# Kernel optimization log

Measured on AMD Instinct MI355X. Metric: run time of the kernel, lower is better.

The kernel has to match this reference:

```python
import jax, jax.numpy as jnp
import numpy as np

H, D = 16, 64  # num_head, num_out
LN_EPS = 1e-5

def setup_inputs() -> dict:
    key = jax.random.key(0)
    ks = jax.random.split(key, 6)
    B, S, C = 4, 2048, 1024
    sc = 0.02
    return {
        "x": jax.random.normal(ks[0], (B, S, C), jnp.float32),
        "mask": jax.random.randint(ks[1], (B, S), 0, 2, jnp.int32),
        "Wq": jax.random.normal(ks[2], (C, C), jnp.float32) * sc,
        "Wk": jax.random.normal(ks[3], (C, C), jnp.float32) * sc,
        "Wv": jax.random.normal(ks[4], (C, C), jnp.float32) * sc,
        "Wr": jax.random.normal(ks[5], (C, C), jnp.float32) * sc,
        "gamma": jnp.ones((C,), jnp.float32),
        "beta": jnp.zeros((C,), jnpip := jnp.float32) if False else jnp.zeros((C,), jnp.float32),
    }

def reference(x, mask, Wq, Wk, Wv, Wr, gamma, beta):
    B, S, C = x.shape
    # torch Linear: y = x @ W.T ; split(num_out,-1) == reshape (B,S,H,D)
    q = (x @ Wq.T).reshape(B, S, H, D)
    k = (x @ Wk.T).reshape(B, S, H, D)
    v = (x @ Wv.T).reshape(B, S, H, D)
    scores = jnp.einsum("bqhd,bkhd->bhqk", q, k) / jnp.sqrt(jnp.float32(D))
    # mask [B,S] over keys; masked positions -> -1e9 (matches masked_fill)
    scores = jnp.where((mask == 0)[:, None, None, :], jnp.float32(-1e9), scores)
    attn = jax.nn.softmax(scores, axis=-1)
    out = jnp.einsum("bhqk,bkhd->bqhd", attn, v).reshape(B, S, H * D)
    out = jax.nn.relu(out + x @ Wr.T)
    mu = jnp.mean(out, axis=-1, keepdims=True)
    var = jnp.mean(jnp.square(out - mu), axis=-1, keepdims=True)
    return (out - mu) / jnp.sqrt(var + LN_EPS) * gamma + beta
```

## Files before the change

kernel.cpp:

```cpp
#include <hip/hip_runtime.h>

typedef __attribute__((ext_vector_type(8))) short short8;
typedef __attribute__((ext_vector_type(8))) unsigned short u16x8;
typedef __attribute__((ext_vector_type(4))) float f32x4;
typedef __attribute__((ext_vector_type(4))) unsigned short u16x4;
typedef __attribute__((ext_vector_type(4))) float float4v;

#define MFMA(a, b, c) __builtin_amdgcn_mfma_f32_16x16x32_bf16(a, b, c, 0, 0, 0)
#define GLOAD_LDS16(gp, lp) __builtin_amdgcn_global_load_lds( \
    (const __attribute__((address_space(1))) void*)(gp),      \
    (__attribute__((address_space(3))) void*)(lp), 16, 0, 0)

__device__ __forceinline__ float bf2f(unsigned short u) {
    union { unsigned int i; float f; } v; v.i = ((unsigned int)u) << 16; return v.f;
}
__device__ __forceinline__ unsigned short f2bf(float f) {
    union { float f; unsigned int i; } v; v.f = f;
    unsigned int r = (v.i + 0x7FFFu + ((v.i >> 16) & 1u)) >> 16;
    return (unsigned short)r;
}
__device__ __forceinline__ unsigned short f2bfr(float f) {
    union { float f; unsigned int i; } v; v.f = f;
    return (unsigned short)((v.i + 0x8000u) >> 16);
}

__global__ __launch_bounds__(256)
void mask_scan(const int* __restrict__ mask, int* __restrict__ kidx, int* __restrict__ seff)
{
    constexpr int S = 2048;
    const int b = blockIdx.x;
    const int tid = threadIdx.x;
    __shared__ int ps[256];
    const int* m = mask + b * S;
    int loc[8], s = 0;
#pragma unroll
    for (int j = 0; j < 8; ++j) { loc[j] = m[tid * 8 + j]; s += loc[j]; }
#pragma unroll
    for (int j = 0; j < 8; ++j) kidx[b * S + tid * 8 + j] = b * S;
    ps[tid] = s;
    __syncthreads();
    for (int off = 1; off < 256; off <<= 1) {
        int v = (tid >= off) ? ps[tid - off] : 0;
        __syncthreads();
        ps[tid] += v;
        __syncthreads();
    }
    int run = (tid > 0) ? ps[tid - 1] : 0;
#pragma unroll
    for (int j = 0; j < 8; ++j) {
        if (loc[j]) kidx[b * S + run] = b * S + tid * 8 + j;
        run += loc[j];
    }
    if (tid == 255) seff[b] = ps[255];
}

__global__ __launch_bounds__(256)
void ingest_all(const float* __restrict__ X,
                const float* __restrict__ Wq, const float* __restrict__ Wk,
                const float* __restrict__ Wv, const float* __restrict__ Wr,
                unsigned short* __restrict__ dst)
{
    constexpr int X4 = 2097152;
    constexpr int T4 = X4 + 4 * 262144;
    const int stride = gridDim.x * blockDim.x;
    for (int i = blockIdx.x * blockDim.x + threadIdx.x; i < T4; i += stride) {
        const float* src;
        int off;
        if (i < X4) { src = X; off = i; }
        else {
            int jj = i - X4;
            int ws = jj >> 18;
            off = jj & 0x3FFFF;
            src = (ws == 0) ? Wq : (ws == 1) ? Wk : (ws == 2) ? Wv : Wr;
        }
        float4v v = ((const float4v*)src)[off];
        u16x4 o;
#pragma unroll
        for (int j = 0; j < 4; ++j) o[j] = f2bf(v[j]);
        ((u16x4*)dst)[i] = o;
    }
}

__global__ __launch_bounds__(256)
void proj_gemm(const unsigned short* __restrict__ X,
               const unsigned short* __restrict__ Wq, const unsigned short* __restrict__ Wk,
               const unsigned short* __restrict__ Wv, const unsigned short* __restrict__ Wr,
               unsigned short* __restrict__ Qo, unsigned short* __restrict__ Ko,
               unsigned short* __restrict__ Vo, unsigned short* __restrict__ Ro,
               const int* __restrict__ kidx, const int* __restrict__ seff)
{
    constexpr int Kd = 1024, N = 1024;
    __shared__ unsigned short smem[128 * 136];
    unsigned short* As = smem;
    unsigned short* Bs = smem + 4096;
    unsigned short* Ct = smem;
    const int tid = threadIdx.x;
    const int wid = tid >> 6, lane = tid & 63;
    const int g = lane >> 4, lr = lane & 15;
    const int bid = blockIdx.x;
    const int jx = bid & 7, t = bid >> 3;
    const int x = (t >> 5) * 8 + jx;
    const int c = t & 31;
    const int wsel = c >> 3;
    const int coltile = c & 7;
    const bool compact = (wsel == 1) || (wsel == 2);
    int rowBase;
    if (compact) {
        if (x >= 68) return;
        int b = x / 17, xt = x - b * 17;
        if (xt * 128 >= seff[b]) return;
        rowBase = b * 2048 + xt * 128;
    } else {
        if (x >= 64) return;
        rowBase = x * 128;
    }
    const unsigned short* W = (wsel == 0) ? Wq : (wsel == 1) ? Wk : (wsel == 2) ? Wv : Wr;
    unsigned short* O = (wsel == 0) ? Qo : (wsel == 1) ? Ko : (wsel == 2) ? Vo : Ro;
    const int colBase = coltile * 128;
    const int wm = wid >> 1, wn = wid & 1;

    f32x4 acc[4][4] = {};

    const int r0 = tid >> 2;
    const int c0 = (tid & 3) * 8;
    const int sA0 = compact ? kidx[rowBase + r0] : rowBase + r0;
    const int sA1 = compact ? kidx[rowBase + 64 + r0] : rowBase + 64 + r0;
    const unsigned short* ga0 = X + (size_t)sA0 * Kd + c0;
    const unsigned short* ga1 = X + (size_t)sA1 * Kd + c0;
    const unsigned short* gb0 = W + (size_t)(colBase + r0) * Kd + c0;
    const unsigned short* gb1 = W + (size_t)(colBase + 64 + r0) * Kd + c0;

    for (int kt = 0; kt < Kd; kt += 32) {
        if (kt) __syncthreads();
        GLOAD_LDS16(ga0 + kt, As + (size_t)tid * 8);
        GLOAD_LDS16(ga1 + kt, As + 2048 + (size_t)tid * 8);
        GLOAD_LDS16(gb0 + kt, Bs + (size_t)tid * 8);
        GLOAD_LDS16(gb1 + kt, Bs + 2048 + (size_t)tid * 8);
        asm volatile("s_waitcnt vmcnt(0)" ::: "memory");
        __syncthreads();
        short8 a[4], b[4];
#pragma unroll
        for (int mt = 0; mt < 4; ++mt)
            a[mt] = *reinterpret_cast<const short8*>(&As[(wm * 64 + mt * 16 + lr) * 32 + g * 8]);
#pragma unroll
        for (int nt = 0; nt < 4; ++nt)
            b[nt] = *reinterpret_cast<const short8*>(&Bs[(wn * 64 + nt * 16 + lr) * 32 + g * 8]);
#pragma unroll
        for (int mt = 0; mt < 4; ++mt)
#pragma unroll
            for (int nt = 0; nt < 4; ++nt)
                acc[mt][nt] = MFMA(a[mt], b[nt], acc[mt][nt]);
    }
    __syncthreads();
#pragma unroll
    for (int mt = 0; mt < 4; ++mt)
#pragma unroll
        for (int nt = 0; nt < 4; ++nt)
#pragma unroll
            for (int r = 0; r < 4; ++r)
                Ct[(wm * 64 + mt * 16 + g * 4 + r) * 136 + wn * 64 + nt * 16 + lr] =
                    f2bf(acc[mt][nt][r]);
    __syncthreads();
#pragma unroll
    for (int pp = 0; pp < 8; ++pp) {
        int row = pp * 16 + (tid >> 4);
        int col = (tid & 15) * 8;
        u16x8 v8 = *reinterpret_cast<const u16x8*>(&Ct[row * 136 + col]);
        *reinterpret_cast<u16x8*>(&O[(size_t)(rowBase + row) * N + colBase + col]) = v8;
    }
}

__global__ __launch_bounds__(512)
void attn_fwd(const unsigned short* __restrict__ Q, const unsigned short* __restrict__ Kb,
              const unsigned short* __restrict__ Vb, const int* __restrict__ seff,
              unsigned short* __restrict__ AO)
{
    constexpr int S = 2048, C = 1024, Dh = 64;
    constexpr int PST = 64;
    constexpr float SCL = 0.125f * 1.44269504f;
    constexpr float FM  = 16.0f;
    constexpr float MSK = -1.0e30f;
    __shared__ unsigned short Kt[2][64 * 64];
    __shared__ unsigned short Vt[2][64 * 64];
    __shared__ unsigned short Pt[8][16 * PST];
    const int tid = threadIdx.x;
    const int w = tid >> 6, lane = tid & 63;
    const int g = lane >> 4, lr = lane & 15;
    const int lin = blockIdx.x;
    const int hb = lin & 63, qt = lin >> 6;
    const int h = hb >> 2, b = hb & 3;
    const int qbase = qt * 128;
    const int qrow = qbase + w * 16 + lr;

    const int Sb = seff[b];
    const int ntiles = (Sb + 63) >> 6;

    const unsigned short* qptr = Q + (size_t)(b * S + qrow) * C + h * Dh;
    short8 qf[2];
    qf[0] = *reinterpret_cast<const short8*>(qptr + g * 8);
    qf[1] = *reinterpret_cast<const short8*>(qptr + 32 + g * 8);

    short8 ones;
#pragma unroll
    for (int j = 0; j < 8; ++j) ones[j] = (short)0x3F80;

    f32x4 o[4] = {};
    f32x4 lacc = {};

    const unsigned short* kg = Kb + (size_t)(b * S) * C + h * Dh;
    const unsigned short* vg = Vb + (size_t)(b * S) * C + h * Dh;

    const int kk0 = tid >> 3;
    const int kd0 = ((tid & 7) ^ (kk0 & 7)) * 8;
    const int vkey = tid >> 3;
    const int vsd = (tid & 7) * 8;

    short8 vv;
    GLOAD_LDS16(kg + (size_t)kk0 * C + kd0, &Kt[0][(size_t)tid * 8]);
    vv = *reinterpret_cast<const short8*>(vg + (size_t)vkey * C + vsd);
    asm volatile("s_waitcnt vmcnt(0)" ::: "memory");
    {
        const unsigned short* bb = (const unsigned short*)&vv;
#pragma unroll
        for (int j = 0; j < 8; ++j) {
            int d = vsd + j;
            int sw = (d & 7) ^ ((d >> 3) & 7);
            Vt[0][d * 64 + ((((vkey >> 3) ^ sw) << 3) | (vkey & 7))] = bb[j];
        }
    }
    __syncthreads();

    int cur = 0;
    for (int tt = 0; tt < ntiles; ++tt) {
        const int t = tt * 64;
        const bool hasNext = (tt + 1) < ntiles;
        if (hasNext) {
            const int tn = t + 64;
            GLOAD_LDS16(kg + (size_t)(tn + kk0) * C + kd0, &Kt[cur ^ 1][(size_t)tid * 8]);
            vv = *reinterpret_cast<const short8*>(vg + (size_t)(tn + vkey) * C + vsd);
        }
        f32x4 s[4];
        __builtin_amdgcn_s_setprio(1);
#pragma unroll
        for (int nt = 0; nt < 4; ++nt) {
            int key = nt * 16 + lr;
            f32x4 a = {};
#pragma unroll
            for (int c = 0; c < 2; ++c) {
                int dd = c * 32 + g * 8;
                short8 kf = *reinterpret_cast<const short8*>(
                    &Kt[cur][key * 64 + (((dd >> 3) ^ (key & 7)) << 3)]);
                a = MFMA(qf[c], kf, a);
            }
            s[nt] = a;
        }
        __builtin_amdgcn_s_setprio(0);
        float madd[4];
#pragma unroll
        for (int nt = 0; nt < 4; ++nt)
            madd[nt] = ((t + nt * 16 + lr) < Sb) ? -FM : MSK;
        unsigned short* Pw = Pt[w];
#pragma unroll
        for (int nt = 0; nt < 4; ++nt) {
            int k = nt * 16 + lr;
#pragma unroll
            for (int r = 0; r < 4; ++r) {
                float p = __builtin_amdgcn_exp2f(s[nt][r] * SCL + madd[nt]);
                int row = g * 4 + r;
                Pw[row * PST + ((((k >> 3) ^ (row & 7)) << 3) | (k & 7))] = f2bfr(p);
            }
        }
        asm volatile("s_waitcnt lgkmcnt(0)" ::: "memory");
        __builtin_amdgcn_sched_barrier(0);
        short8 pf[2];
#pragma unroll
        for (int hh = 0; hh < 2; ++hh) {
            int kk = hh * 32 + g * 8;
            pf[hh] = *reinterpret_cast<const short8*>(
                &Pw[lr * PST + (((kk >> 3) ^ (lr & 7)) << 3)]);
        }
        __builtin_amdgcn_s_setprio(1);
        lacc = MFMA(pf[0], ones, lacc);
        lacc = MFMA(pf[1], ones, lacc);
#pragma unroll
        for (int dt = 0; dt < 4; ++dt) {
            int d = dt * 16 + lr;
#pragma unroll
            for (int hh = 0; hh < 2; ++hh) {
                int kk = hh * 32 + g * 8;
                short8 vf = *reinterpret_cast<const short8*>(
                    &Vt[cur][d * 64 + ((((kk >> 3) ^ (d & 7) ^ ((d >> 3) & 7)) << 3))]);
                o[dt] = MFMA(pf[hh], vf, o[dt]);
            }
        }
        __builtin_amdgcn_s_setprio(0);
        if (hasNext) {
            asm volatile("s_waitcnt vmcnt(0)" ::: "memory");
            const unsigned short* bb = (const unsigned short*)&vv;
            unsigned short* Vn = Vt[cur ^ 1];
#pragma unroll
            for (int j = 0; j < 8; ++j) {
                int d = vsd + j;
                int sw = (d & 7) ^ ((d >> 3) & 7);
                Vn[d * 64 + ((((vkey >> 3) ^ sw) << 3) | (vkey & 7))] = bb[j];
            }
        }
        __syncthreads();
        cur ^= 1;
    }
#pragma unroll
    for (int dt = 0; dt < 4; ++dt)
#pragma unroll
        for (int r = 0; r < 4; ++r) {
            int row = qbase + w * 16 + g * 4 + r;
            int col = h * Dh + dt * 16 + lr;
            AO[(size_t)(b * S + row) * C + col] = f2bf(o[dt][r] / lacc[r]);
        }
}

__global__ __launch_bounds__(256)
void ln_ep(const unsigned short* __restrict__ AO, const unsigned short* __restrict__ R,
           const float* __restrict__ gamma, const float* __restrict__ beta,
           float* __restrict__ out)
{
    constexpr int C = 1024;
    const int row = blockIdx.x;
    const int tid = threadIdx.x;
    __shared__ float red[4][2];

    float v[4]; float sum = 0.f, ss = 0.f;
    u16x4 av = *reinterpret_cast<const u16x4*>(AO + (size_t)row * C + tid * 4);
    u16x4 rv = *reinterpret_cast<const u16x4*>(R + (size_t)row * C + tid * 4);
#pragma unroll
    for (int i = 0; i < 4; ++i) {
        v[i] = fmaxf(0.f, bf2f(av[i]) + bf2f(rv[i]));
        sum += v[i]; ss += v[i] * v[i];
    }
#pragma unroll
    for (int off = 1; off < 64; off <<= 1) {
        sum += __shfl_xor(sum, off, 64);
        ss += __shfl_xor(ss, off, 64);
    }
    int w = tid >> 6;
    if ((tid & 63) == 0) { red[w][0] = sum; red[w][1] = ss; }
    __syncthreads();
    sum = red[0][0] + red[1][0] + red[2][0] + red[3][0];
    ss = red[0][1] + red[1][1] + red[2][1] + red[3][1];
    float mu = sum * (1.f / C);
    float var = ss * (1.f / C) - mu * mu;
    float rstd = rsqrtf(var + 1e-5f);
    float4v g4 = *reinterpret_cast<const float4v*>(gamma + tid * 4);
    float4v b4 = *reinterpret_cast<const float4v*>(beta + tid * 4);
    float4v ov;
#pragma unroll
    for (int i = 0; i < 4; ++i)
        ov[i] = (v[i] - mu) * rstd * g4[i] + b4[i];
    *reinterpret_cast<float4v*>(out + (size_t)row * C + tid * 4) = ov;
}

extern "C" void kernel_launch(void* const* d_in, const int* in_sizes, int n_in,
                              void* d_out, int out_size, void* d_ws, size_t ws_size,
                              hipStream_t stream)
{
    const float* X = (const float*)d_in[0];
    const int* mask = (const int*)d_in[1];
    const float* Wq = (const float*)d_in[2];
    const float* Wk = (const float*)d_in[3];
    const float* Wv = (const float*)d_in[4];
    const float* Wr = (const float*)d_in[5];
    const float* Gm = (const float*)d_in[6];
    const float* Bt = (const float*)d_in[7];
    float* out = (float*)d_out;

    const size_t NE = (size_t)8192 * 1024;
    const size_t WE = (size_t)1024 * 1024;
    unsigned short* p = (unsigned short*)d_ws;
    unsigned short* Xb = p;   p += NE;
    unsigned short* Wqb = p;  p += WE;
    unsigned short* Wkb = p;  p += WE;
    unsigned short* Wvb = p;  p += WE;
    unsigned short* Wrb = p;  p += WE;
    unsigned short* Qb = p;   p += NE;
    unsigned short* Kb = p;   p += NE;
    unsigned short* Vb = p;   p += NE;
    unsigned short* Rb = p;   p += NE;
    int* kidx = (int*)p;      p += 8192 * 2;
    int* seff = (int*)p;      p += 8;
    unsigned short* AO = Xb;

    mask_scan<<<dim3(4), 256, 0, stream>>>(mask, kidx, seff);
    ingest_all<<<dim3(2048), 256, 0, stream>>>(X, Wq, Wk, Wv, Wr, Xb);

    proj_gemm<<<dim3(2304), 256, 0, stream>>>(Xb, Wqb, Wkb, Wvb, Wrb,
                                              Qb, Kb, Vb, Rb, kidx, seff);
    attn_fwd<<<dim3(1024), 512, 0, stream>>>(Qb, Kb, Vb, seff, AO);
    ln_ep<<<dim3(8192), 256, 0, stream>>>(AO, Rb, Gm, Bt, out);
}
```

Measured before the change: 172.9 us.

## Double K-tile depth in projection GEMM and XOR-swizzle LDS layout

```diff
diff --git a/kernel.cpp b/kernel.cpp
--- a/kernel.cpp
+++ b/kernel.cpp
@@ -92,7 +92,7 @@
     constexpr int Kd = 1024, N = 1024;
     __shared__ unsigned short smem[128 * 136];
     unsigned short* As = smem;
-    unsigned short* Bs = smem + 4096;
+    unsigned short* Bs = smem + 8192;
     unsigned short* Ct = smem;
     const int tid = threadIdx.x;
     const int wid = tid >> 6, lane = tid & 63;
@@ -121,35 +121,49 @@
 
     f32x4 acc[4][4] = {};
 
-    const int r0 = tid >> 2;
-    const int c0 = (tid & 3) * 8;
-    const int sA0 = compact ? kidx[rowBase + r0] : rowBase + r0;
-    const int sA1 = compact ? kidx[rowBase + 64 + r0] : rowBase + 64 + r0;
-    const unsigned short* ga0 = X + (size_t)sA0 * Kd + c0;
-    const unsigned short* ga1 = X + (size_t)sA1 * Kd + c0;
-    const unsigned short* gb0 = W + (size_t)(colBase + r0) * Kd + c0;
-    const unsigned short* gb1 = W + (size_t)(colBase + 64 + r0) * Kd + c0;
-
-    for (int kt = 0; kt < Kd; kt += 32) {
+    const unsigned short* srcA[4];
+    const unsigned short* srcB[4];
+#pragma unroll
+    for (int i = 0; i < 4; ++i) {
+        int n = tid + 256 * i;
+        int r = n >> 3;
+        int cb = (n & 7) ^ (r & 7);
+        int sA = compact ? kidx[rowBase + r] : rowBase + r;
+        srcA[i] = X + (size_t)sA * Kd + cb * 8;
+        srcB[i] = W + (size_t)(colBase + r) * Kd + cb * 8;
+    }
+
+    for (int kt = 0; kt < Kd; kt += 64) {
         if (kt) __syncthreads();
-        GLOAD_LDS16(ga0 + kt, As + (size_t)tid * 8);
-        GLOAD_LDS16(ga1 + kt, As + 2048 + (size_t)tid * 8);
-        GLOAD_LDS16(gb0 + kt, Bs + (size_t)tid * 8);
-        GLOAD_LDS16(gb1 + kt, Bs + 2048 + (size_t)tid * 8);
+#pragma unroll
+        for (int i = 0; i < 4; ++i)
+            GLOAD_LDS16(srcA[i] + kt, As + (size_t)(tid + 256 * i) * 8);
+#pragma unroll
+        for (int i = 0; i < 4; ++i)
+            GLOAD_LDS16(srcB[i] + kt, Bs + (size_t)(tid + 256 * i) * 8);
         asm volatile("s_waitcnt vmcnt(0)" ::: "memory");
         __syncthreads();
-        short8 a[4], b[4];
-#pragma unroll
-        for (int mt = 0; mt < 4; ++mt)
-            a[mt] = *reinterpret_cast<const short8*>(&As[(wm * 64 + mt * 16 + lr) * 32 + g * 8]);
-#pragma unroll
-        for (int nt = 0; nt < 4; ++nt)
-            b[nt] = *reinterpret_cast<const short8*>(&Bs[(wn * 64 + nt * 16 + lr) * 32 + g * 8]);
-#pragma unroll
-        for (int mt = 0; mt < 4; ++mt)
-#pragma unroll
-            for (int nt = 0; nt < 4; ++nt)
-                acc[mt][nt] = MFMA(a[mt], b[nt], acc[mt][nt]);
+#pragma unroll
+        for (int kkb = 0; kkb < 8; kkb += 4) {
+            short8 a[4], b[4];
+#pragma unroll
+            for (int mt = 0; mt < 4; ++mt) {
+                int row = wm * 64 + mt * 16 + lr;
+                a[mt] = *reinterpret_cast<const short8*>(
+                    &As[row * 64 + (((g + kkb) ^ (lr & 7)) << 3)]);
+            }
+#pragma unroll
+            for (int nt = 0; nt < 4; ++nt) {
+                int row = wn * 64 + nt * 16 + lr;
+                b[nt] = *reinterpret_cast<const short8*>(
+                    &Bs[row * 64 + (((g + kkb) ^ (lr & 7)) << 3)]);
+            }
+#pragma unroll
+            for (int mt = 0; mt < 4; ++mt)
+#pragma unroll
+                for (int nt = 0; nt < 4; ++nt)
+                    acc[mt][nt] = MFMA(a[mt], b[nt], acc[mt][nt]);
+        }
     }
     __syncthreads();
 #pragma unroll
```

Measured after the change: 165.1 us. 1.05x faster.
